# Optimization experiments

Measured on AMD Instinct MI355X. Metric: run time of the kernel, lower is better.

Reference implementation:

```python
import jax, jax.numpy as jnp
import numpy as np

H = 6144  # canvas_shape[0]
W = 6144  # canvas_shape[1]
LINE_WIDTH = 1.0


def setup_inputs() -> dict:
    key = jax.random.key(0)
    k0, k1 = jax.random.split(key)
    p0 = jax.random.uniform(k0, (2,), dtype=jnp.float32)
    p1 = jax.random.uniform(k1, (2,), dtype=jnp.float32)
    return {"p0": p0, "p1": p1}


def reference(p0, p1):
    # Scale normalized endpoints to pixel coordinates (same as torch.tensor(canvas_shape) mult).
    shape_vec = jnp.array([H, W], dtype=jnp.float32)
    p0 = p0 * shape_vec
    p1 = p1 * shape_vec
    d = p1 - p0                              # p1_minus_p0, shape [2]
    len_sq = d[0] ** 2 + d[1] ** 2           # squared segment length (scalar)

    # Original loops: canvas[x, y] evaluated at point p = (x, y).
    # x indexes the first canvas axis, y the second (square canvas).
    X = jnp.arange(H, dtype=jnp.float32)[:, None]   # [H, 1] -> p_x
    Y = jnp.arange(W, dtype=jnp.float32)[None, :]   # [1, W] -> p_y

    px = X - p0[0]                           # (p - p0)_x, broadcasts to [H, W]
    py = Y - p0[1]
    t = jnp.clip((px * d[0] + py * d[1]) / len_sq, 0.0, 1.0)  # [H, W]
    proj_x = p0[0] + t * d[0]
    proj_y = p0[1] + t * d[1]
    dist = jnp.sqrt((X - proj_x) ** 2 + (Y - proj_y) ** 2)    # [H, W]

    canvas = jnp.where(dist < LINE_WIDTH, LINE_WIDTH - dist, jnp.float32(0.0))
    return canvas
```

## Files before the change

kernel.cpp:

```cpp
#include <hip/hip_runtime.h>

#define CANVAS_H 6144
#define CANVAS_W 6144
#define BLOCK 256
#define PER_THREAD 16
#define WAVE_PX (64 * PER_THREAD)
#define BLOCK_PX (BLOCK * PER_THREAD)

typedef float f32x4 __attribute__((ext_vector_type(4)));

__global__ __launch_bounds__(BLOCK) void
LineRaster2d_kernel(const float* __restrict__ p0g,
                    const float* __restrict__ p1g,
                    float* __restrict__ out) {
    const int lane   = threadIdx.x & 63;
    const int waveId = blockIdx.x * (BLOCK / 64) + (threadIdx.x >> 6);
    const int wbase  = waveId * WAVE_PX;

    const int x  = (int)((unsigned)wbase / CANVAS_W);
    const int yw = wbase - x * CANVAS_W;

    const float p0x = p0g[0] * (float)CANVAS_H;
    const float p0y = p0g[1] * (float)CANVAS_W;
    const float dx  = p1g[0] * (float)CANVAS_H - p0x;
    const float dy  = p1g[1] * (float)CANVAS_W - p0y;
    const float inv_len_sq = __builtin_amdgcn_rcpf(dx * dx + dy * dy);

    const float px    = (float)x - p0x;
    const float px_dx = px * dx;

    #pragma unroll
    for (int j = 0; j < PER_THREAD / 4; ++j) {
        const int y0 = yw + j * 256 + lane * 4;

        f32x4 r = (f32x4)(0.0f, 0.0f, 0.0f, 0.0f);

        const float pyc = ((float)y0 + 1.5f) - p0y;
        float tc = (px_dx + pyc * dy) * inv_len_sq;
        tc = fminf(fmaxf(tc, 0.0f), 1.0f);
        const float ecx = px - tc * dx;
        const float ecy = pyc - tc * dy;

        if (ecx * ecx + ecy * ecy < 9.0f) {
            float py, t, ex, ey, dist;

            py = (float)(y0 + 0) - p0y;
            t  = fminf(fmaxf((px_dx + py * dy) * inv_len_sq, 0.0f), 1.0f);
            ex = px - t * dx;  ey = py - t * dy;
            dist = __builtin_amdgcn_sqrtf(ex * ex + ey * ey);
            r.x = (dist < 1.0f) ? (1.0f - dist) : 0.0f;

            py = (float)(y0 + 1) - p0y;
            t  = fminf(fmaxf((px_dx + py * dy) * inv_len_sq, 0.0f), 1.0f);
            ex = px - t * dx;  ey = py - t * dy;
            dist = __builtin_amdgcn_sqrtf(ex * ex + ey * ey);
            r.y = (dist < 1.0f) ? (1.0f - dist) : 0.0f;

            py = (float)(y0 + 2) - p0y;
            t  = fminf(fmaxf((px_dx + py * dy) * inv_len_sq, 0.0f), 1.0f);
            ex = px - t * dx;  ey = py - t * dy;
            dist = __builtin_amdgcn_sqrtf(ex * ex + ey * ey);
            r.z = (dist < 1.0f) ? (1.0f - dist) : 0.0f;

            py = (float)(y0 + 3) - p0y;
            t  = fminf(fmaxf((px_dx + py * dy) * inv_len_sq, 0.0f), 1.0f);
            ex = px - t * dx;  ey = py - t * dy;
            dist = __builtin_amdgcn_sqrtf(ex * ex + ey * ey);
            r.w = (dist < 1.0f) ? (1.0f - dist) : 0.0f;
        }

        __builtin_nontemporal_store(
            r, reinterpret_cast<f32x4*>(out + wbase + j * 256 + lane * 4));
    }
}

extern "C" void kernel_launch(void* const* d_in, const int* in_sizes, int n_in,
                              void* d_out, int out_size, void* d_ws, size_t ws_size,
                              hipStream_t stream) {
    const float* p0 = (const float*)d_in[0];
    const float* p1 = (const float*)d_in[1];
    float* out = (float*)d_out;

    const long long n_pix = (long long)CANVAS_H * CANVAS_W;
    const int n_blocks = (int)(n_pix / BLOCK_PX);

    LineRaster2d_kernel<<<n_blocks, BLOCK, 0, stream>>>(p0, p1, out);
}
```

Before: 155.3 us.

## Switch to persistent grid-stride loop over quads with plain stores

Replaces the one-shot grid of small blocks with a fixed 2048-block persistent grid. Each thread walks quads in a grid-stride loop and updates row and column incrementally instead of dividing each time. Nontemporal stores are swapped for ordinary vector stores. The aim is to cut block launch and scheduling overhead on a write-bound kernel. The trade-offs are a serial loop per thread and possibly different cache write behaviour.

```diff
diff --git a/kernel.cpp b/kernel.cpp
--- a/kernel.cpp
+++ b/kernel.cpp
@@ -3,9 +3,12 @@
 #define CANVAS_H 6144
 #define CANVAS_W 6144
 #define BLOCK 256
-#define PER_THREAD 16
-#define WAVE_PX (64 * PER_THREAD)
-#define BLOCK_PX (BLOCK * PER_THREAD)
+#define GRID 2048
+#define NTHREADS (GRID * BLOCK)
+#define NQUADS ((CANVAS_H * CANVAS_W) / 4)
+#define STEPS (NQUADS / NTHREADS)
+#define ROW_ADV 341
+#define COL_ADV 2048
 
 typedef float f32x4 __attribute__((ext_vector_type(4)));
 
@@ -13,12 +16,7 @@
 LineRaster2d_kernel(const float* __restrict__ p0g,
                     const float* __restrict__ p1g,
                     float* __restrict__ out) {
-    const int lane   = threadIdx.x & 63;
-    const int waveId = blockIdx.x * (BLOCK / 64) + (threadIdx.x >> 6);
-    const int wbase  = waveId * WAVE_PX;
-
-    const int x  = (int)((unsigned)wbase / CANVAS_W);
-    const int yw = wbase - x * CANVAS_W;
+    const int tid = blockIdx.x * BLOCK + threadIdx.x;
 
     const float p0x = p0g[0] * (float)CANVAS_H;
     const float p0y = p0g[1] * (float)CANVAS_W;
@@ -26,14 +24,16 @@
     const float dy  = p1g[1] * (float)CANVAS_W - p0y;
     const float inv_len_sq = __builtin_amdgcn_rcpf(dx * dx + dy * dy);
 
-    const float px    = (float)x - p0x;
-    const float px_dx = px * dx;
+    int q   = tid;
+    const int px0 = q * 4;
+    int x   = (int)((unsigned)px0 / CANVAS_W);
+    int y0  = px0 - x * CANVAS_W;
 
-    #pragma unroll
-    for (int j = 0; j < PER_THREAD / 4; ++j) {
-        const int y0 = yw + j * 256 + lane * 4;
+    for (int s = 0; s < STEPS; ++s) {
+        f32x4 r = (f32x4)(0.0f, 0.0f, 0.0f, 0.0f);
 
-        f32x4 r = (f32x4)(0.0f, 0.0f, 0.0f, 0.0f);
+        const float px    = (float)x - p0x;
+        const float px_dx = px * dx;
 
         const float pyc = ((float)y0 + 1.5f) - p0y;
         float tc = (px_dx + pyc * dy) * inv_len_sq;
@@ -69,8 +69,12 @@
             r.w = (dist < 1.0f) ? (1.0f - dist) : 0.0f;
         }
 
-        __builtin_nontemporal_store(
-            r, reinterpret_cast<f32x4*>(out + wbase + j * 256 + lane * 4));
+        *reinterpret_cast<f32x4*>(out + (size_t)q * 4) = r;
+
+        q  += NTHREADS;
+        x  += ROW_ADV;
+        y0 += COL_ADV;
+        if (y0 >= CANVAS_W) { y0 -= CANVAS_W; x += 1; }
     }
 }
 
@@ -81,8 +85,5 @@
     const float* p1 = (const float*)d_in[1];
     float* out = (float*)d_out;
 
-    const long long n_pix = (long long)CANVAS_H * CANVAS_W;
-    const int n_blocks = (int)(n_pix / BLOCK_PX);
-
-    LineRaster2d_kernel<<<n_blocks, BLOCK, 0, stream>>>(p0, p1, out);
+    LineRaster2d_kernel<<<GRID, BLOCK, 0, stream>>>(p0, p1, out);
 }
```

Measured after the change: 153.1 us. Within noise of the previous version (-1.4%).
